# Optimization experiments

Hardware: AMD Instinct MI355X
Metric: run time of the kernel (lower is better)

## Reference

```python
import jax, jax.numpy as jnp
import numpy as np

B, S, E, H = 4, 2048, 1024, 16
D = E // H  # head_dim


def setup_inputs() -> dict:
    key = jax.random.key(0)
    ks = jax.random.split(key, 5)
    scale = 1.0 / np.sqrt(E)
    return {
        "qkv": jax.random.normal(ks[0], (B, S, E), jnp.float32),
        "in_w": jax.random.normal(ks[1], (3 * E, E), jnp.float32) * scale,
        "in_b": jax.random.normal(ks[2], (3 * E,), jnp.float32) * scale,
        "out_w": jax.random.normal(ks[3], (E, E), jnp.float32) * scale,
        "out_b": jax.random.normal(ks[4], (E,), jnp.float32) * scale,
    }


def reference(qkv, in_w, in_b, out_w, out_b):
    # in_proj: torch Linear -> x @ W^T + b, output [B,S,3E]
    x1 = jnp.einsum('bse,fe->bsf', qkv, in_w) + in_b
    q, k, v = jnp.split(x1, 3, axis=2)  # each [B,S,E]
    # reshape to heads: [B,H,S,D] (contiguous head_dim slices == reshape)
    q = q.reshape(B, S, H, D).transpose(0, 2, 1, 3)
    k = k.reshape(B, S, H, D).transpose(0, 2, 1, 3)
    v = v.reshape(B, S, H, D).transpose(0, 2, 1, 3)
    scores = jnp.einsum('bhqd,bhkd->bhqk', q, k) / jnp.sqrt(jnp.float32(D))
    attn = jax.nn.softmax(scores, axis=-1)  # dropout p=0.0 -> identity
    out = jnp.einsum('bhqk,bhkd->bhqd', attn, v)  # [B,H,S,D]
    out = out.transpose(0, 2, 1, 3).reshape(B, S, E)
    return jnp.einsum('bse,fe->bsf', out, out_w) + out_b
```

## Files before the change

### kernel.cpp

```cpp
#include <hip/hip_runtime.h>


typedef __attribute__((ext_vector_type(8))) short s16x8;
typedef __attribute__((ext_vector_type(8))) __bf16 bf16x8;
typedef __attribute__((ext_vector_type(4))) float f32x4;
typedef __attribute__((ext_vector_type(16))) float f32x16;
typedef __attribute__((ext_vector_type(4))) unsigned short u16x4;
typedef __attribute__((ext_vector_type(4))) unsigned int u32x4;

#define QSCALE_F 0.18033688011112042f

#if __has_builtin(__builtin_amdgcn_exp2f)
#define EXP2F(x) __builtin_amdgcn_exp2f(x)
#else
#define EXP2F(x) exp2f(x)
#endif

__device__ __forceinline__ unsigned short f2bf(float f) {
  unsigned int u = __builtin_bit_cast(unsigned int, f);
  u += 0x7fffu + ((u >> 16) & 1u);
  return (unsigned short)(u >> 16);
}

__device__ __forceinline__ f32x4 mfma16(s16x8 a, s16x8 b, f32x4 c) {
  return __builtin_amdgcn_mfma_f32_16x16x32_bf16(
      __builtin_bit_cast(bf16x8, a), __builtin_bit_cast(bf16x8, b), c, 0, 0, 0);
}
__device__ __forceinline__ f32x16 mfma32(s16x8 a, s16x8 b, f32x16 c) {
  return __builtin_amdgcn_mfma_f32_32x32x16_bf16(
      __builtin_bit_cast(bf16x8, a), __builtin_bit_cast(bf16x8, b), c, 0, 0, 0);
}

__device__ __forceinline__ unsigned cvtpk(float lo, float hi) {
  unsigned r;
  asm("v_cvt_pk_bf16_f32 %0, %1, %2" : "=v"(r) : "v"(lo), "v"(hi));
  return r;
}
__device__ __forceinline__ void p32swap(unsigned &a, unsigned &b) {
  asm volatile("v_permlane32_swap_b32 %0, %1" : "+v"(a), "+v"(b));
}

#define GLL16(gp, lp) __builtin_amdgcn_global_load_lds(                       \
    (const __attribute__((address_space(1))) void*)(gp),                      \
    (__attribute__((address_space(3))) void*)(lp), 16, 0, 0)

#define SBAR0 __builtin_amdgcn_sched_barrier(0)
#define HWBAR __builtin_amdgcn_s_barrier()
#define LGKM0 asm volatile("s_waitcnt lgkmcnt(0)" ::: "memory")
#define VMC5 asm volatile("s_waitcnt vmcnt(5)" ::: "memory")
#define VMC2 asm volatile("s_waitcnt vmcnt(2)" ::: "memory")
#define VMC0 asm volatile("s_waitcnt vmcnt(0)" ::: "memory")
#define PRIO1 __builtin_amdgcn_s_setprio(1)
#define PRIO0 __builtin_amdgcn_s_setprio(0)

__global__ void cvt_f32_bf16(const float* __restrict__ in,
                             unsigned short* __restrict__ out,
                             int n, int scale_n) {
  int idx = (blockIdx.x * 256 + threadIdx.x) * 4;
  int stride = gridDim.x * 256 * 4;
  for (int i = idx; i < n; i += stride) {
    const float4 v = *reinterpret_cast<const float4*>(in + i);
    const float sc = (i < scale_n) ? QSCALE_F : 1.0f;
    u16x4 r;
    r.x = f2bf(v.x * sc); r.y = f2bf(v.y * sc);
    r.z = f2bf(v.z * sc); r.w = f2bf(v.w * sc);
    *reinterpret_cast<u16x4*>(out + i) = r;
  }
}

__global__ __launch_bounds__(512, 2) void gemm1_8ph(
    const unsigned short* __restrict__ A, const unsigned short* __restrict__ B,
    const float* __restrict__ bias, unsigned short* __restrict__ C,
    int M, int N, int K, int qscale_cols) {
  __shared__ __align__(16) unsigned short As[2][256 * 64];
  __shared__ __align__(16) unsigned short Bs[2][192 * 64];
  const int NT = K >> 6;
  const int id = blockIdx.x;
  const int xc = id & 7, r0 = id >> 3;
  const int mi_ = xc * 4 + (r0 & 3);
  const int ni_ = r0 >> 2;
  const int bm = mi_ * 256, bn = ni_ * 192;

  const int tid = threadIdx.x;
  const int lane = tid & 63, w = tid >> 6;
  const int l15 = lane & 15, l4 = (lane >> 4) & 3;
  const int wm = w >> 2, wn = w & 3;
  const int swz = (l15 & 7) << 4;

#define STG_U(ldsc_, gb_, unit_, ktel_) {                                     \
    const int o = (unit_) * 8192 + tid * 16;                                  \
    const int row_ = o >> 7;                                                  \
    const int cb_ = (o & 127) ^ ((row_ & 7) << 4);                            \
    GLL16((gb_) + (size_t)row_ * K + (ktel_) + (cb_ >> 1),                    \
          (char*)(ldsc_) + o);                                                \
  }
#define RD_A(buf_, qm_, dst_) {                                               \
    _Pragma("unroll") for (int mt = 0; mt < 4; ++mt)                          \
      _Pragma("unroll") for (int kk = 0; kk < 2; ++kk)                        \
        dst_[mt][kk] = *(const s16x8*)((const char*)As[buf_] +                \
            (wm * 128 + (qm_) * 64 + mt * 16 + l15) * 128 +                   \
            ((kk * 64 + l4 * 16) ^ swz));                                     \
  }
#define RD_B01(buf_, dst_) {                                                  \
    _Pragma("unroll") for (int nt = 0; nt < 2; ++nt)                          \
      _Pragma("unroll") for (int kk = 0; kk < 2; ++kk)                        \
        dst_[nt][kk] = *(const s16x8*)((const char*)Bs[buf_] +                \
            (wn * 48 + nt * 16 + l15) * 128 +                                 \
            ((kk * 64 + l4 * 16) ^ swz));                                     \
  }
#define RD_B2(buf_, dst_) {                                                   \
    _Pragma("unroll") for (int kk = 0; kk < 2; ++kk)                          \
      dst_[kk] = *(const s16x8*)((const char*)Bs[buf_] +                      \
          (wn * 48 + 32 + l15) * 128 + ((kk * 64 + l4 * 16) ^ swz));          \
  }
#define MM16(qm_) {                                                           \
    _Pragma("unroll") for (int mt = 0; mt < 4; ++mt)                          \
      _Pragma("unroll") for (int nt = 0; nt < 2; ++nt)                        \
        _Pragma("unroll") for (int kk = 0; kk < 2; ++kk)                      \
          acc[(qm_) * 4 + mt][nt] = mfma16(                                   \
              a[mt][kk], b01[nt][kk], acc[(qm_) * 4 + mt][nt]);               \
  }
#define MM8(qm_) {                                                            \
    _Pragma("unroll") for (int mt = 0; mt < 4; ++mt)                          \
      _Pragma("unroll") for (int kk = 0; kk < 2; ++kk)                        \
        acc[(qm_) * 4 + mt][2] = mfma16(                                      \
            a[mt][kk], b2[kk], acc[(qm_) * 4 + mt][2]);                       \
  }

  f32x4 acc[8][3];
#pragma unroll
  for (int i = 0; i < 8; ++i)
#pragma unroll
    for (int j = 0; j < 3; ++j) acc[i][j] = (f32x4){0.f, 0.f, 0.f, 0.f};

  const unsigned short* Ag = A + (size_t)bm * K;
  const unsigned short* Bg = B + (size_t)bn * K;

  STG_U(Bs[0], Bg, 0, 0); STG_U(Bs[0], Bg, 1, 0); STG_U(Bs[0], Bg, 2, 0);
  STG_U(As[0], Ag, 0, 0); STG_U(As[0], Ag, 2, 0);
  STG_U(As[0], Ag, 1, 0); STG_U(As[0], Ag, 3, 0);
  VMC0;
  SBAR0; HWBAR;

  s16x8 a[4][2], b01[2][2], b2[2];
  for (int t = 0; t < NT; ++t) {
    const int cur = t & 1, oth = cur ^ 1;
    const bool st = (t + 1 < NT);
    const int kel = (t + 1) * 64;
    RD_A(cur, 0, a);
    RD_B01(cur, b01);
    if (st) { STG_U(Bs[oth], Bg, 0, kel); STG_U(Bs[oth], Bg, 1, kel);
              STG_U(Bs[oth], Bg, 2, kel); }
    SBAR0; HWBAR; LGKM0; SBAR0;
    PRIO1; MM16(0); PRIO0;
    SBAR0; HWBAR;
    RD_B2(cur, b2);
    if (st) { STG_U(As[oth], Ag, 0, kel); STG_U(As[oth], Ag, 2, kel); }
    SBAR0; HWBAR; LGKM0; SBAR0;
    PRIO1; MM8(0); PRIO0;
    SBAR0;
    if (st) { VMC5; } else { VMC0; }
    HWBAR;
    RD_A(cur, 1, a);
    if (st) { STG_U(As[oth], Ag, 1, kel); STG_U(As[oth], Ag, 3, kel); }
    SBAR0; HWBAR; LGKM0; SBAR0;
    PRIO1; MM8(1); PRIO0;
    SBAR0; HWBAR;
    PRIO1; MM16(1); PRIO0;
    SBAR0;
    if (st) { VMC2; } else { VMC0; }
    HWBAR;
  }

#pragma unroll
  for (int mi = 0; mi < 8; ++mi)
#pragma unroll
    for (int ni = 0; ni < 3; ++ni) {
      const int col = bn + wn * 48 + ni * 16 + l15;
      const float bsc = (col < qscale_cols) ? QSCALE_F : 1.0f;
      const float bv = bias[col] * bsc;
#pragma unroll
      for (int r = 0; r < 4; ++r) {
        const int row = bm + wm * 128 + mi * 16 + l4 * 4 + r;
        C[(size_t)row * N + col] = f2bf(acc[mi][ni][r] + bv);
      }
    }
#undef STG_U
#undef RD_A
#undef RD_B01
#undef RD_B2
#undef MM16
#undef MM8
}

template <bool OUT_BF16>
__global__ __launch_bounds__(256, 2) void gemm_nt(
    const unsigned short* __restrict__ A, const unsigned short* __restrict__ B,
    const float* __restrict__ bias, void* __restrict__ Cout,
    int M, int N, int K, int qscale_cols) {
  __shared__ __align__(16) unsigned short As[128 * 64];
  __shared__ __align__(16) unsigned short Bs[128 * 64];
  const int tid = threadIdx.x;
  const int lane = tid & 63, w = tid >> 6;
  const int l15 = lane & 15, l4 = lane >> 4;
  const int wr = w >> 1, wc = w & 1;
  const int bm = blockIdx.y * 128, bn = blockIdx.x * 128;

  f32x4 acc[4][4];
#pragma unroll
  for (int i = 0; i < 4; ++i)
#pragma unroll
    for (int j = 0; j < 4; ++j) acc[i][j] = (f32x4){0.f, 0.f, 0.f, 0.f};

  for (int kt = 0; kt < K; kt += 64) {
#pragma unroll
    for (int j = 0; j < 4; ++j) {
      const int gb = (j * 4 + w) * 64;
      const int g = gb + lane;
      const int row = g >> 3, seg = g & 7;
      GLL16(A + (size_t)(bm + row) * K + kt + seg * 8, As + gb * 8);
      GLL16(B + (size_t)(bn + row) * K + kt + seg * 8, Bs + gb * 8);
    }
    __syncthreads();
#pragma unroll
    for (int kk = 0; kk < 2; ++kk) {
      s16x8 a[4], b[4];
#pragma unroll
      for (int mi = 0; mi < 4; ++mi)
        a[mi] = *reinterpret_cast<const s16x8*>(
            As + (wr * 64 + mi * 16 + l15) * 64 + kk * 32 + l4 * 8);
#pragma unroll
      for (int ni = 0; ni < 4; ++ni)
        b[ni] = *reinterpret_cast<const s16x8*>(
            Bs + (wc * 64 + ni * 16 + l15) * 64 + kk * 32 + l4 * 8);
#pragma unroll
      for (int mi = 0; mi < 4; ++mi)
#pragma unroll
        for (int ni = 0; ni < 4; ++ni)
          acc[mi][ni] = mfma16(a[mi], b[ni], acc[mi][ni]);
    }
    __syncthreads();
  }
#pragma unroll
  for (int mi = 0; mi < 4; ++mi) {
#pragma unroll
    for (int ni = 0; ni < 4; ++ni) {
      const int col = bn + wc * 64 + ni * 16 + l15;
      const float bsc = (col < qscale_cols) ? QSCALE_F : 1.0f;
      const float bv = bias[col] * bsc;
#pragma unroll
      for (int r = 0; r < 4; ++r) {
        const int row = bm + wr * 64 + mi * 16 + l4 * 4 + r;
        const float val = acc[mi][ni][r] + bv;
        if (OUT_BF16)
          ((unsigned short*)Cout)[(size_t)row * N + col] = f2bf(val);
        else
          ((float*)Cout)[(size_t)row * N + col] = val;
      }
    }
  }
}

__global__ __launch_bounds__(256, 4) void attn_fwd(
    const unsigned short* __restrict__ X1, unsigned short* __restrict__ O) {
  __shared__ __align__(16) unsigned short Ks[2][64 * 64];
  __shared__ __align__(16) unsigned short Vt[2][64 * 64];

  const int id = blockIdx.x;
  const int xc = id & 7, r0 = id >> 3;
  const int bh = xc * 8 + (r0 & 7);
  const int qt = r0 >> 3;
  const int b = bh >> 4, h = bh & 15;
  const int tid = threadIdx.x;
  const int lane = tid & 63, w = tid >> 6;
  const int l31 = lane & 31, hi = lane >> 5;

  const unsigned short* Qp = X1 + (size_t)b * 2048 * 3072 + h * 64;
  const unsigned short* Kp = Qp + 1024;
  const unsigned short* Vp = Qp + 2048;
  const int q0 = qt * 128 + w * 32;

  s16x8 qf[4];
#pragma unroll
  for (int kk = 0; kk < 4; ++kk)
    qf[kk] = *reinterpret_cast<const s16x8*>(
        Qp + (size_t)(q0 + l31) * 3072 + kk * 16 + hi * 8);

  f32x16 oacc[2];
#pragma unroll
  for (int db = 0; db < 2; ++db)
#pragma unroll
    for (int i = 0; i < 16; ++i) oacc[db][i] = 0.f;
  float l_r = 0.f;

#define STAGE_K(kt_, buf_)                                                    \
  {                                                                           \
    _Pragma("unroll") for (int j = 0; j < 2; ++j) {                           \
      const int chunk = (j * 4 + w) * 1024;                                   \
      const int o = chunk + lane * 16;                                        \
      const int row = o >> 7;                                                 \
      const int srcb = (o & 127) ^ ((row & 7) << 4);                          \
      GLL16(Kp + (size_t)((kt_) + row) * 3072 + (srcb >> 1),                  \
            (char*)Ks[buf_] + chunk);                                         \
    }                                                                         \
  }
#define LOAD_V(kt_, vr_)                                                      \
  {                                                                           \
    _Pragma("unroll") for (int j = 0; j < 2; ++j) {                           \
      const int seg = w + 4 * j;                                              \
      vr_[j] = *reinterpret_cast<const s16x8*>(                               \
          Vp + (size_t)((kt_) + lane) * 3072 + seg * 8);                      \
    }                                                                         \
  }
#define WRITE_V(vr_, buf_)                                                    \
  {                                                                           \
    _Pragma("unroll") for (int j = 0; j < 2; ++j) {                           \
      const int seg = w + 4 * j;                                              \
      _Pragma("unroll") for (int e = 0; e < 8; ++e) {                         \
        const int d = seg * 8 + e;                                            \
        const int byt = d * 128 + ((lane * 2) ^ (e << 4));                    \
        *(unsigned short*)((char*)Vt[buf_] + byt) = (unsigned short)vr_[j][e];\
      }                                                                       \
    }                                                                         \
  }

  s16x8 vnxt[2];
  LOAD_V(0, vnxt);
  STAGE_K(0, 0);
  WRITE_V(vnxt, 0);
  __syncthreads();

  for (int t = 0; t < 32; ++t) {
    const int cur = t & 1;
    const unsigned short* Ksc = Ks[cur];
    const unsigned short* Vtc = Vt[cur];
    if (t < 31) {
      LOAD_V((t + 1) * 64, vnxt);
      STAGE_K((t + 1) * 64, cur ^ 1);
    }

    f32x16 sa[2];
#pragma unroll
    for (int sub = 0; sub < 2; ++sub)
#pragma unroll
      for (int i = 0; i < 16; ++i) sa[sub][i] = 0.f;
    PRIO1;
#pragma unroll
    for (int sub = 0; sub < 2; ++sub) {
      const int row = sub * 32 + l31;
#pragma unroll
      for (int kk = 0; kk < 4; ++kk) {
        const int byt = row * 128 + ((kk * 32 + hi * 16) ^ ((l31 & 7) << 4));
        s16x8 ka = *reinterpret_cast<const s16x8*>((const char*)Ksc + byt);
        sa[sub] = mfma32(ka, qf[kk], sa[sub]);
      }
    }
    PRIO0;

    float s0 = 0.f, s1 = 0.f, s2 = 0.f, s3 = 0.f;
#pragma unroll
    for (int sub = 0; sub < 2; ++sub)
#pragma unroll
      for (int i = 0; i < 16; i += 4) {
        sa[sub][i]     = EXP2F(sa[sub][i]);     s0 += sa[sub][i];
        sa[sub][i + 1] = EXP2F(sa[sub][i + 1]); s1 += sa[sub][i + 1];
        sa[sub][i + 2] = EXP2F(sa[sub][i + 2]); s2 += sa[sub][i + 2];
        sa[sub][i + 3] = EXP2F(sa[sub][i + 3]); s3 += sa[sub][i + 3];
      }
    float rsum = (s0 + s1) + (s2 + s3);
    rsum += __shfl_xor(rsum, 32);
    l_r += rsum;

    s16x8 pa[2][2];
#pragma unroll
    for (int sub = 0; sub < 2; ++sub)
#pragma unroll
      for (int g = 0; g < 2; ++g) {
        unsigned c0 = cvtpk(sa[sub][g * 8 + 0], sa[sub][g * 8 + 1]);
        unsigned c1 = cvtpk(sa[sub][g * 8 + 2], sa[sub][g * 8 + 3]);
        unsigned c2 = cvtpk(sa[sub][g * 8 + 4], sa[sub][g * 8 + 5]);
        unsigned c3 = cvtpk(sa[sub][g * 8 + 6], sa[sub][g * 8 + 7]);
        p32swap(c0, c2);
        p32swap(c1, c3);
        u32x4 tt = {c0, c1, c2, c3};
        pa[sub][g] = __builtin_bit_cast(s16x8, tt);
      }

    PRIO1;
#pragma unroll
    for (int db = 0; db < 2; ++db) {
      const int row = db * 32 + l31;
#pragma unroll
      for (int sub = 0; sub < 2; ++sub)
#pragma unroll
        for (int g = 0; g < 2; ++g) {
          const int byt =
              row * 128 + (((sub * 2 + g) * 32 + hi * 16) ^ ((l31 & 7) << 4));
          s16x8 vb = *reinterpret_cast<const s16x8*>((const char*)Vtc + byt);
          oacc[db] = mfma32(pa[sub][g], vb, oacc[db]);
        }
    }
    PRIO0;

    if (t < 31) WRITE_V(vnxt, cur ^ 1);
    __syncthreads();
  }

  const float invl = 1.0f / l_r;
#pragma unroll
  for (int r = 0; r < 16; ++r) {
    const int crow = (r & 3) + 8 * (r >> 2) + 4 * hi;
    const float ir = __shfl(invl, crow);
    const size_t base = (size_t)(b * 2048 + q0 + crow) * 1024 + h * 64 + l31;
    O[base] = f2bf(oacc[0][r] * ir);
    O[base + 32] = f2bf(oacc[1][r] * ir);
  }
}

extern "C" void kernel_launch(void* const* d_in, const int* in_sizes, int n_in,
                              void* d_out, int out_size, void* d_ws,
                              size_t ws_size, hipStream_t stream) {
  const float* qkv   = (const float*)d_in[0];
  const float* in_w  = (const float*)d_in[1];
  const float* in_b  = (const float*)d_in[2];
  const float* out_w = (const float*)d_in[3];
  const float* out_b = (const float*)d_in[4];
  float* out = (float*)d_out;
  char* ws = (char*)d_ws;

  unsigned short* qkv_bf  = (unsigned short*)(ws);
  unsigned short* win_bf  = (unsigned short*)(ws + 16777216);
  unsigned short* wout_bf = (unsigned short*)(ws + 23068672);
  unsigned short* x1      = (unsigned short*)(ws + 25165824);
  unsigned short* attn_out = qkv_bf;

  cvt_f32_bf16<<<2048, 256, 0, stream>>>(qkv, qkv_bf, 8388608, 0);
  cvt_f32_bf16<<<1024, 256, 0, stream>>>(in_w, win_bf, 3145728, 1048576);
  cvt_f32_bf16<<<512, 256, 0, stream>>>(out_w, wout_bf, 1048576, 0);

  gemm1_8ph<<<512, 512, 0, stream>>>(
      qkv_bf, win_bf, in_b, x1, 8192, 3072, 1024, 1024);

  attn_fwd<<<1024, 256, 0, stream>>>(x1, attn_out);

  gemm_nt<false><<<dim3(8, 64), 256, 0, stream>>>(
      attn_out, wout_bf, out_b, (void*)out, 8192, 1024, 1024, 0);
}
```

Baseline: 190.6 us.

## Process two 32-row query subtiles per wave to reuse K/V fragments

Each wave in the attention kernel now handles 64 query rows instead of 32, as two subtiles. K and V fragments are loaded from LDS once per tile and reused for both subtiles, halving LDS traffic per MFMA and halving how often each K/V tile is staged. In exchange, register use roughly doubles for accumulators, scores and Q fragments, so launch bounds drop to 2 and the grid is halved to 512 blocks. That lowers occupancy and the number of blocks per CU.

```diff
diff --git a/kernel.cpp b/kernel.cpp
--- a/kernel.cpp
+++ b/kernel.cpp
@@ -261,7 +261,7 @@
   }
 }
 
-__global__ __launch_bounds__(256, 4) void attn_fwd(
+__global__ __launch_bounds__(256, 2) void attn_fwd(
     const unsigned short* __restrict__ X1, unsigned short* __restrict__ O) {
   __shared__ __align__(16) unsigned short Ks[2][64 * 64];
   __shared__ __align__(16) unsigned short Vt[2][64 * 64];
@@ -278,20 +278,24 @@
   const unsigned short* Qp = X1 + (size_t)b * 2048 * 3072 + h * 64;
   const unsigned short* Kp = Qp + 1024;
   const unsigned short* Vp = Qp + 2048;
-  const int q0 = qt * 128 + w * 32;
-
-  s16x8 qf[4];
-#pragma unroll
-  for (int kk = 0; kk < 4; ++kk)
-    qf[kk] = *reinterpret_cast<const s16x8*>(
-        Qp + (size_t)(q0 + l31) * 3072 + kk * 16 + hi * 8);
-
-  f32x16 oacc[2];
-#pragma unroll
-  for (int db = 0; db < 2; ++db)
-#pragma unroll
-    for (int i = 0; i < 16; ++i) oacc[db][i] = 0.f;
-  float l_r = 0.f;
+  const int q0 = qt * 256 + w * 64;
+
+  s16x8 qf[2][4];
+#pragma unroll
+  for (int qs = 0; qs < 2; ++qs)
+#pragma unroll
+    for (int kk = 0; kk < 4; ++kk)
+      qf[qs][kk] = *reinterpret_cast<const s16x8*>(
+          Qp + (size_t)(q0 + qs * 32 + l31) * 3072 + kk * 16 + hi * 8);
+
+  f32x16 oacc[2][2];
+#pragma unroll
+  for (int qs = 0; qs < 2; ++qs)
+#pragma unroll
+    for (int db = 0; db < 2; ++db)
+#pragma unroll
+      for (int i = 0; i < 16; ++i) oacc[qs][db][i] = 0.f;
+  float l_r[2] = {0.f, 0.f};
 
 #define STAGE_K(kt_, buf_)                                                    \
   {                                                                           \
@@ -339,81 +343,103 @@
       STAGE_K((t + 1) * 64, cur ^ 1);
     }
 
-    f32x16 sa[2];
-#pragma unroll
-    for (int sub = 0; sub < 2; ++sub)
-#pragma unroll
-      for (int i = 0; i < 16; ++i) sa[sub][i] = 0.f;
-    PRIO1;
+    s16x8 kf[2][4];
 #pragma unroll
     for (int sub = 0; sub < 2; ++sub) {
       const int row = sub * 32 + l31;
 #pragma unroll
       for (int kk = 0; kk < 4; ++kk) {
         const int byt = row * 128 + ((kk * 32 + hi * 16) ^ ((l31 & 7) << 4));
-        s16x8 ka = *reinterpret_cast<const s16x8*>((const char*)Ksc + byt);
-        sa[sub] = mfma32(ka, qf[kk], sa[sub]);
+        kf[sub][kk] = *reinterpret_cast<const s16x8*>((const char*)Ksc + byt);
       }
     }
+    f32x16 sa[2][2];
+#pragma unroll
+    for (int qs = 0; qs < 2; ++qs)
+#pragma unroll
+      for (int sub = 0; sub < 2; ++sub)
+#pragma unroll
+        for (int i = 0; i < 16; ++i) sa[qs][sub][i] = 0.f;
+    PRIO1;
+#pragma unroll
+    for (int qs = 0; qs < 2; ++qs)
+#pragma unroll
+      for (int sub = 0; sub < 2; ++sub)
+#pragma unroll
+        for (int kk = 0; kk < 4; ++kk)
+          sa[qs][sub] = mfma32(kf[sub][kk], qf[qs][kk], sa[qs][sub]);
     PRIO0;
 
-    float s0 = 0.f, s1 = 0.f, s2 = 0.f, s3 = 0.f;
-#pragma unroll
-    for (int sub = 0; sub < 2; ++sub)
-#pragma unroll
-      for (int i = 0; i < 16; i += 4) {
-        sa[sub][i]     = EXP2F(sa[sub][i]);     s0 += sa[sub][i];
-        sa[sub][i + 1] = EXP2F(sa[sub][i + 1]); s1 += sa[sub][i + 1];
-        sa[sub][i + 2] = EXP2F(sa[sub][i + 2]); s2 += sa[sub][i + 2];
-        sa[sub][i + 3] = EXP2F(sa[sub][i + 3]); s3 += sa[sub][i + 3];
-      }
-    float rsum = (s0 + s1) + (s2 + s3);
-    rsum += __shfl_xor(rsum, 32);
-    l_r += rsum;
-
-    s16x8 pa[2][2];
-#pragma unroll
-    for (int sub = 0; sub < 2; ++sub)
-#pragma unroll
-      for (int g = 0; g < 2; ++g) {
-        unsigned c0 = cvtpk(sa[sub][g * 8 + 0], sa[sub][g * 8 + 1]);
-        unsigned c1 = cvtpk(sa[sub][g * 8 + 2], sa[sub][g * 8 + 3]);
-        unsigned c2 = cvtpk(sa[sub][g * 8 + 4], sa[sub][g * 8 + 5]);
-        unsigned c3 = cvtpk(sa[sub][g * 8 + 6], sa[sub][g * 8 + 7]);
-        p32swap(c0, c2);
-        p32swap(c1, c3);
-        u32x4 tt = {c0, c1, c2, c3};
-        pa[sub][g] = __builtin_bit_cast(s16x8, tt);
-      }
-
-    PRIO1;
+    s16x8 pa[2][2][2];
+#pragma unroll
+    for (int qs = 0; qs < 2; ++qs) {
+      float s0 = 0.f, s1 = 0.f, s2 = 0.f, s3 = 0.f;
+#pragma unroll
+      for (int sub = 0; sub < 2; ++sub)
+#pragma unroll
+        for (int i = 0; i < 16; i += 4) {
+          sa[qs][sub][i]     = EXP2F(sa[qs][sub][i]);     s0 += sa[qs][sub][i];
+          sa[qs][sub][i + 1] = EXP2F(sa[qs][sub][i + 1]); s1 += sa[qs][sub][i + 1];
+          sa[qs][sub][i + 2] = EXP2F(sa[qs][sub][i + 2]); s2 += sa[qs][sub][i + 2];
+          sa[qs][sub][i + 3] = EXP2F(sa[qs][sub][i + 3]); s3 += sa[qs][sub][i + 3];
+        }
+      float rsum = (s0 + s1) + (s2 + s3);
+      rsum += __shfl_xor(rsum, 32);
+      l_r[qs] += rsum;
+#pragma unroll
+      for (int sub = 0; sub < 2; ++sub)
+#pragma unroll
+        for (int g = 0; g < 2; ++g) {
+          unsigned c0 = cvtpk(sa[qs][sub][g * 8 + 0], sa[qs][sub][g * 8 + 1]);
+          unsigned c1 = cvtpk(sa[qs][sub][g * 8 + 2], sa[qs][sub][g * 8 + 3]);
+          unsigned c2 = cvtpk(sa[qs][sub][g * 8 + 4], sa[qs][sub][g * 8 + 5]);
+          unsigned c3 = cvtpk(sa[qs][sub][g * 8 + 6], sa[qs][sub][g * 8 + 7]);
+          p32swap(c0, c2);
+          p32swap(c1, c3);
+          u32x4 tt = {c0, c1, c2, c3};
+          pa[qs][sub][g] = __builtin_bit_cast(s16x8, tt);
+        }
+    }
+
+    s16x8 vb[2][4];
 #pragma unroll
     for (int db = 0; db < 2; ++db) {
       const int row = db * 32 + l31;
 #pragma unroll
-      for (int sub = 0; sub < 2; ++sub)
-#pragma unroll
-        for (int g = 0; g < 2; ++g) {
-          const int byt =
-              row * 128 + (((sub * 2 + g) * 32 + hi * 16) ^ ((l31 & 7) << 4));
-          s16x8 vb = *reinterpret_cast<const s16x8*>((const char*)Vtc + byt);
-          oacc[db] = mfma32(pa[sub][g], vb, oacc[db]);
-        }
-    }
+      for (int ks = 0; ks < 4; ++ks) {
+        const int byt = row * 128 + ((ks * 32 + hi * 16) ^ ((l31 & 7) << 4));
+        vb[db][ks] = *reinterpret_cast<const s16x8*>((const char*)Vtc + byt);
+      }
+    }
+    PRIO1;
+#pragma unroll
+    for (int qs = 0; qs < 2; ++qs)
+#pragma unroll
+      for (int db = 0; db < 2; ++db)
+#pragma unroll
+        for (int sub = 0; sub < 2; ++sub)
+#pragma unroll
+          for (int g = 0; g < 2; ++g)
+            oacc[qs][db] =
+                mfma32(pa[qs][sub][g], vb[db][sub * 2 + g], oacc[qs][db]);
     PRIO0;
 
     if (t < 31) WRITE_V(vnxt, cur ^ 1);
     __syncthreads();
   }
 
-  const float invl = 1.0f / l_r;
-#pragma unroll
-  for (int r = 0; r < 16; ++r) {
-    const int crow = (r & 3) + 8 * (r >> 2) + 4 * hi;
-    const float ir = __shfl(invl, crow);
-    const size_t base = (size_t)(b * 2048 + q0 + crow) * 1024 + h * 64 + l31;
-    O[base] = f2bf(oacc[0][r] * ir);
-    O[base + 32] = f2bf(oacc[1][r] * ir);
+#pragma unroll
+  for (int qs = 0; qs < 2; ++qs) {
+    const float invl = 1.0f / l_r[qs];
+#pragma unroll
+    for (int r = 0; r < 16; ++r) {
+      const int crow = (r & 3) + 8 * (r >> 2) + 4 * hi;
+      const float ir = __shfl(invl, crow);
+      const size_t base =
+          (size_t)(b * 2048 + q0 + qs * 32 + crow) * 1024 + h * 64 + l31;
+      O[base] = f2bf(oacc[qs][0][r] * ir);
+      O[base + 32] = f2bf(oacc[qs][1][r] * ir);
+    }
   }
 }
 
@@ -441,7 +467,7 @@
   gemm1_8ph<<<512, 512, 0, stream>>>(
       qkv_bf, win_bf, in_b, x1, 8192, 3072, 1024, 1024);
 
-  attn_fwd<<<1024, 256, 0, stream>>>(x1, attn_out);
+  attn_fwd<<<512, 256, 0, stream>>>(x1, attn_out);
 
   gemm_nt<false><<<dim3(8, 64), 256, 0, stream>>>(
       attn_out, wout_bf, out_b, (void*)out, 8192, 1024, 1024, 0);
```

New measurement: 187.6 us. About the same (-1.6%).
